# Performance work log

Measured on AMD Instinct MI355X. Metric: run time of the kernel, lower is better.

Reference implementation:

```python
import jax, jax.numpy as jnp
import numpy as np

H_DIM = 64
GRID = 8
NBR = 2.0
BN_EPS = 1e-5
N_SEQ = 64
N_PED = 64
BOTTLENECK = 1024


def setup_inputs() -> dict:
    key = jax.random.key(0)
    k0, k1, k2, k3 = jax.random.split(key, 4)
    batch = N_SEQ * N_PED
    h_states = jax.random.normal(k0, (1, batch, H_DIM), jnp.float32)
    # positions spread over a 4x4 area so some neighbors fall inside the 2.0 neighborhood
    end_pos = jax.random.uniform(k1, (batch, 2), jnp.float32) * 4.0
    rel_pos = jax.random.normal(k2, (batch, 2), jnp.float32)
    starts = jnp.arange(N_SEQ, dtype=jnp.int32) * N_PED
    seq_start_end = jnp.stack([starts, starts + N_PED], axis=1)
    in_dim = GRID * GRID * H_DIM  # 4096
    W = jax.random.normal(k3, (in_dim, BOTTLENECK), jnp.float32) / np.sqrt(in_dim)
    b = jnp.zeros((BOTTLENECK,), jnp.float32)
    gamma = jnp.ones((BOTTLENECK,), jnp.float32)
    beta = jnp.zeros((BOTTLENECK,), jnp.float32)
    return {"h_states": h_states, "seq_start_end": seq_start_end, "end_pos": end_pos,
            "rel_pos": rel_pos, "W": W, "b": b, "gamma": gamma, "beta": beta}


def _pool_scene(hidden, pos):
    # hidden: (n, h), pos: (n, 2). Pair (i, j): ped j binned into ped i's grid.
    n, h = hidden.shape
    g2 = GRID * GRID
    half = NBR / 2.0
    tl_x = pos[:, 0] - half
    tl_y = pos[:, 1] + half
    br_x = pos[:, 0] + half
    br_y = pos[:, 1] - half
    px = pos[None, :, 0]  # (1, n) -> broadcast over i
    py = pos[None, :, 1]
    cell_x = jnp.floor((px - tl_x[:, None]) / NBR * GRID)
    cell_y = jnp.floor((tl_y[:, None] - py) / NBR * GRID)
    grid = (cell_x + cell_y * GRID).astype(jnp.int32) + 1  # slot 0 = trash bin
    oob = ((px >= br_x[:, None]) | (px <= tl_x[:, None]) |
           (py >= tl_y[:, None]) | (py <= br_y[:, None]) |
           jnp.eye(n, dtype=bool))  # self-interaction excluded
    grid = grid + (jnp.arange(n, dtype=jnp.int32) * g2)[:, None]
    grid = jnp.where(oob, 0, grid)  # (n, n)
    src = jnp.broadcast_to(hidden[None], (n, n, h)).reshape(-1, h)
    buf = jnp.zeros((n * g2 + 1, h), hidden.dtype).at[grid.reshape(-1)].add(src)
    return buf[1:].reshape(n, g2 * h)


def reference(h_states, seq_start_end, end_pos, rel_pos, W, b, gamma, beta):
    batch = end_pos.shape[0]
    n_seq = seq_start_end.shape[0]
    n_ped = batch // n_seq  # equal-length scenes by construction
    hid = h_states.reshape(-1, H_DIM).reshape(n_seq, n_ped, H_DIM)
    pos = end_pos.reshape(n_seq, n_ped, 2)
    pool_h = jax.vmap(_pool_scene)(hid, pos).reshape(batch, -1)  # (batch, 4096)
    x = pool_h @ W + b
    # BatchNorm1d in training mode (batch statistics, biased variance)
    mean = jnp.mean(x, axis=0)
    var = jnp.var(x, axis=0)
    x = (x - mean) * jax.lax.rsqrt(var + BN_EPS) * gamma + beta
    return jax.nn.relu(x)
```

## Files before the change

### kernel.cpp

```cpp
#include <hip/hip_runtime.h>
#include <hip/hip_bf16.h>


#define NPED  64
#define BATCH 4096
#define HDIM  64
#define G2    64
#define KDIM  4096
#define NOUT  1024

typedef __attribute__((ext_vector_type(8))) short short8;
typedef __attribute__((ext_vector_type(4))) float f32x4;

__device__ __forceinline__ unsigned short f2bf(float f) {
    __hip_bfloat16 h = __float2bfloat16(f);
    return *reinterpret_cast<unsigned short*>(&h);
}

__device__ __forceinline__ void lds_load16(const void* g, void* l) {
    __builtin_amdgcn_global_load_lds(
        (const __attribute__((address_space(1))) void*)g,
        (__attribute__((address_space(3))) void*)l, 16, 0, 0);
}

__global__ __launch_bounds__(512) void pool_kernel(const float* __restrict__ h,
                                                   const float* __restrict__ pos,
                                                   unsigned short* __restrict__ A2) {
    __shared__ float hs[NPED * HDIM];
    __shared__ float pl[NPED * 2];
    int t = threadIdx.x;
    int w = t >> 6, lane = t & 63;
    int p0 = blockIdx.x * 8;
    int sbase = p0 & ~(NPED - 1);
    if (t < 128) pl[t] = pos[sbase * 2 + t];
    {
        const float4* src = (const float4*)(h + (size_t)sbase * HDIM);
        float4* dst = (float4*)hs;
        dst[t] = src[t];
        dst[t + 512] = src[t + 512];
    }
    __syncthreads();

    int i = p0 + w;
    int il = i & (NPED - 1);
    float cx0 = pl[2 * il], cy0 = pl[2 * il + 1];
    float tlx = cx0 - 1.f, tly = cy0 + 1.f, brx = cx0 + 1.f, bry = cy0 - 1.f;
    float px = pl[2 * lane], py = pl[2 * lane + 1];
    bool inb = (lane != il) && !(px >= brx || px <= tlx || py >= tly || py <= bry);
    int cellx = (int)floorf((px - tlx) * 4.f);
    int celly = (int)floorf((tly - py) * 4.f);
    int cell = cellx + celly * 8;
    inb = inb && ((unsigned)cell < 64u);

    int mtile = i >> 4, r = i & 15;
    unsigned short* outb = A2 + (size_t)mtile * 65536 + r * 8
                              + (lane >> 5) * 512 + ((lane >> 3) & 3) * 128 + (lane & 7);
    const float* hrow = hs + lane;
    #pragma unroll
    for (int c = 0; c < 64; ++c) {
        unsigned long long m = __ballot(inb && (cell == c));
        float a = 0.f;
        while (m) {
            int j = __builtin_ctzll(m);
            m &= m - 1;
            a += hrow[j * HDIM];
        }
        outb[c * 1024] = f2bf(a);
    }
}

__global__ __launch_bounds__(256) void wt_kernel(const float* __restrict__ W,
                                                 unsigned short* __restrict__ Wt,
                                                 float* __restrict__ stats) {
    __shared__ unsigned short tile[64][66];
    int k0 = blockIdx.x * 64;
    int n0 = blockIdx.y * 64;
    int t = threadIdx.x;
    if (blockIdx.x == 0 && blockIdx.y < 8) stats[blockIdx.y * 256 + t] = 0.f;
    #pragma unroll
    for (int p = 0; p < 4; ++p) {
        int lin = p * 256 + t;
        int c4 = lin & 15, kl = lin >> 4;
        float4 v = ((const float4*)(W + (size_t)(k0 + kl) * NOUT + n0))[c4];
        tile[c4 * 4 + 0][kl] = f2bf(v.x);
        tile[c4 * 4 + 1][kl] = f2bf(v.y);
        tile[c4 * 4 + 2][kl] = f2bf(v.z);
        tile[c4 * 4 + 3][kl] = f2bf(v.w);
    }
    __syncthreads();
    unsigned int* out = (unsigned int*)Wt;
    #pragma unroll
    for (int p = 0; p < 8; ++p) {
        int lin = p * 256 + t;
        int ku = lin & 31, nl = lin >> 5;
        unsigned int v = (unsigned int)tile[nl][2 * ku] |
                         ((unsigned int)tile[nl][2 * ku + 1] << 16);
        out[(size_t)(n0 + nl) * (KDIM / 2) + (k0 >> 1) + ku] = v;
    }
}

__global__ __launch_bounds__(256, 2) void gemm_kernel(const unsigned short* __restrict__ A2,
                                                      const unsigned short* __restrict__ Bt,
                                                      float* __restrict__ C,
                                                      float* __restrict__ P1,
                                                      float* __restrict__ P2,
                                                      float* __restrict__ P3) {
    __shared__ __align__(16) unsigned short Bs[128 * 64];
    int t = threadIdx.x;
    int w = t >> 6, lane = t & 63;
    int m0 = blockIdx.x * 256, n0 = blockIdx.y * 128;
    int kbase = blockIdx.z * 1024;
    int wm = w * 64;

    f32x4 acc[4][8];
    #pragma unroll
    for (int i = 0; i < 4; ++i)
        #pragma unroll
        for (int j = 0; j < 8; ++j)
            acc[i][j] = (f32x4){0.f, 0.f, 0.f, 0.f};

    int rbase = w * 32 + (lane >> 3);
    int koff = ((lane & 7) ^ (lane >> 3)) * 8;
    const unsigned short* Bg = Bt + (size_t)(n0 + rbase) * KDIM + kbase + koff;
    unsigned short* BsW = Bs + w * 2048 + lane * 8;

    const unsigned short* Abase = A2 + (size_t)((m0 + wm) >> 4) * 65536 + lane * 8;
    int ktile0 = kbase >> 5;

    for (int kt = 0; kt < 1024; kt += 64) {
        #pragma unroll
        for (int q = 0; q < 4; ++q)
            lds_load16(Bg + (size_t)q * 8 * KDIM + kt, BsW + q * 512);
        short8 af[2][4];
        int ktile = ktile0 + (kt >> 5);
        #pragma unroll
        for (int kk = 0; kk < 2; ++kk)
            #pragma unroll
            for (int i = 0; i < 4; ++i)
                af[kk][i] = *(const short8*)(Abase + ((size_t)i * 128 + ktile + kk) * 512);
        __syncthreads();
        #pragma unroll
        for (int kk = 0; kk < 2; ++kk) {
            int chunk = ((kk * 4 + (lane >> 4)) ^ (lane & 7)) * 8;
            #pragma unroll
            for (int j = 0; j < 8; ++j) {
                short8 b = *(const short8*)&Bs[(j * 16 + (lane & 15)) * 64 + chunk];
                #pragma unroll
                for (int i = 0; i < 4; ++i)
                    acc[i][j] = __builtin_amdgcn_mfma_f32_16x16x32_bf16(af[kk][i], b, acc[i][j], 0, 0, 0);
            }
        }
        __syncthreads();
    }

    float* dst = blockIdx.z == 0 ? C : blockIdx.z == 1 ? P1 : blockIdx.z == 2 ? P2 : P3;
    int col0 = n0 + (lane & 15);
    int row0 = m0 + wm + ((lane >> 4) << 2);
    #pragma unroll
    for (int i = 0; i < 4; ++i)
        #pragma unroll
        for (int j = 0; j < 8; ++j)
            #pragma unroll
            for (int r = 0; r < 4; ++r)
                dst[(size_t)(row0 + i * 16 + r) * NOUT + col0 + j * 16] = acc[i][j][r];
}

__global__ __launch_bounds__(256) void combine_stats(float* __restrict__ C,
                                                     const float* __restrict__ P1,
                                                     const float* __restrict__ P2,
                                                     const float* __restrict__ P3,
                                                     float* __restrict__ stats) {
    int t = threadIdx.x;
    int colchunk = blockIdx.x & 3;
    int rowchunk = blockIdx.x >> 2;
    int col = colchunk * 256 + t;
    size_t base = (size_t)rowchunk * 32 * NOUT + col;
    float s = 0.f, s2 = 0.f;
    #pragma unroll 4
    for (int r = 0; r < 32; ++r) {
        size_t ix = base + (size_t)r * NOUT;
        float v = (C[ix] + P1[ix]) + (P2[ix] + P3[ix]);
        C[ix] = v;
        s += v; s2 += v * v;
    }
    atomicAdd(&stats[col], s);
    atomicAdd(&stats[NOUT + col], s2);
}

__global__ __launch_bounds__(256) void norm_kernel(float* __restrict__ C,
                                                   const float* __restrict__ stats,
                                                   const float* __restrict__ gamma,
                                                   const float* __restrict__ beta) {
    int idx = blockIdx.x * 256 + threadIdx.x;
    int col4 = idx & 255;
    float4 x = ((const float4*)C)[idx];
    float4 s = ((const float4*)stats)[col4];
    float4 q = ((const float4*)(stats + NOUT))[col4];
    float4 g = ((const float4*)gamma)[col4];
    float4 b = ((const float4*)beta)[col4];
    const float inv_n = 1.f / 4096.f;
    float m, inv;
    m = s.x * inv_n; inv = rsqrtf(q.x * inv_n - m * m + 1e-5f); x.x = fmaxf((x.x - m) * inv * g.x + b.x, 0.f);
    m = s.y * inv_n; inv = rsqrtf(q.y * inv_n - m * m + 1e-5f); x.y = fmaxf((x.y - m) * inv * g.y + b.y, 0.f);
    m = s.z * inv_n; inv = rsqrtf(q.z * inv_n - m * m + 1e-5f); x.z = fmaxf((x.z - m) * inv * g.z + b.z, 0.f);
    m = s.w * inv_n; inv = rsqrtf(q.w * inv_n - m * m + 1e-5f); x.w = fmaxf((x.w - m) * inv * g.w + b.w, 0.f);
    ((float4*)C)[idx] = x;
}

extern "C" void kernel_launch(void* const* d_in, const int* in_sizes, int n_in,
                              void* d_out, int out_size, void* d_ws, size_t ws_size,
                              hipStream_t stream) {
    const float* h      = (const float*)d_in[0];
    const float* endpos = (const float*)d_in[2];
    const float* W      = (const float*)d_in[4];
    const float* gamma  = (const float*)d_in[6];
    const float* beta   = (const float*)d_in[7];
    float* C = (float*)d_out;

    char* ws = (char*)d_ws;
    size_t off = 0;
    unsigned short* A2 = (unsigned short*)(ws + off); off += (size_t)BATCH * KDIM * 2;
    unsigned short* Wt = (unsigned short*)(ws + off); off += (size_t)NOUT * KDIM * 2;
    float* P1 = (float*)(ws + off); off += (size_t)BATCH * NOUT * 4;
    float* P2 = (float*)(ws + off); off += (size_t)BATCH * NOUT * 4;
    float* P3 = (float*)(ws + off); off += (size_t)BATCH * NOUT * 4;
    float* stats = (float*)(ws + off);

    pool_kernel<<<BATCH / 8, 512, 0, stream>>>(h, endpos, A2);
    wt_kernel<<<dim3(KDIM / 64, NOUT / 64), 256, 0, stream>>>(W, Wt, stats);
    gemm_kernel<<<dim3(BATCH / 256, NOUT / 128, 4), 256, 0, stream>>>(A2, Wt, C, P1, P2, P3);
    combine_stats<<<512, 256, 0, stream>>>(C, P1, P2, P3, stats);
    norm_kernel<<<(BATCH * NOUT / 4) / 256, 256, 0, stream>>>(C, stats, gamma, beta);
}
```

Before: 149.9 us.

## Rewrite GEMM as double-buffered 256x256 tile pipeline with XCD-aware block mapping

The split-K GEMM moves from 256x128 tiles with 4 waves to 256x256 tiles with 8 waves. Both A and B are now staged into LDS with double buffering, and the next K-tile's global-to-LDS loads are interleaved with the MFMA quadrants under explicit barriers, waitcnts and setprio. A 1D grid with XCD-aware remapping is meant to keep blocks that share operand panels on the same L2. The goal is to hide memory latency and raise operand reuse, at the cost of 128KB of LDS per block and a heavily hand-scheduled, fragile synchronisation sequence.

```diff
diff --git a/kernel.cpp b/kernel.cpp
--- a/kernel.cpp
+++ b/kernel.cpp
@@ -22,6 +22,14 @@
         (const __attribute__((address_space(1))) void*)g,
         (__attribute__((address_space(3))) void*)l, 16, 0, 0);
 }
+
+#define BAR() do { __builtin_amdgcn_sched_barrier(0); \
+                   __builtin_amdgcn_s_barrier(); \
+                   __builtin_amdgcn_sched_barrier(0); } while (0)
+#define LGKM0() do { asm volatile("s_waitcnt lgkmcnt(0)" ::: "memory"); \
+                     __builtin_amdgcn_sched_barrier(0); } while (0)
+#define VMCNT4() asm volatile("s_waitcnt vmcnt(4)" ::: "memory")
+#define VMCNT0() asm volatile("s_waitcnt vmcnt(0)" ::: "memory")
 
 __global__ __launch_bounds__(512) void pool_kernel(const float* __restrict__ h,
                                                    const float* __restrict__ pos,
@@ -99,67 +107,186 @@
     }
 }
 
-__global__ __launch_bounds__(256, 2) void gemm_kernel(const unsigned short* __restrict__ A2,
+
+__device__ __forceinline__ void stage_A_half(const unsigned short* __restrict__ A2blk,
+                                             unsigned short* AsBuf, int T, int h, int t) {
+    #pragma unroll
+    for (int q = 0; q < 2; ++q) {
+        int s = q * 512 + t;
+        int ml = h * 8 + (s >> 7);
+        int inner = s & 127;
+        lds_load16(A2blk + (size_t)ml * 65536 + T * 1024 + inner * 8,
+                   AsBuf + h * 8192 + s * 8);
+    }
+}
+
+__device__ __forceinline__ void stage_B_half(const unsigned short* __restrict__ Wtblk,
+                                             unsigned short* BsBuf, int T, int h, int t) {
+    #pragma unroll
+    for (int q = 0; q < 2; ++q) {
+        int s = q * 512 + t;
+        int row = h * 128 + (s >> 3);
+        int swz = (s & 7) ^ ((s >> 3) & 7);
+        lds_load16(Wtblk + (size_t)row * KDIM + T * 64 + swz * 8,
+                   BsBuf + h * 8192 + s * 8);
+    }
+}
+
+__device__ __forceinline__ void read_A(short8 (&a)[2][4], const unsigned short* AsBuf,
+                                       int mtbase, int lane) {
+    #pragma unroll
+    for (int i = 0; i < 4; ++i)
+        #pragma unroll
+        for (int kk = 0; kk < 2; ++kk)
+            a[kk][i] = *(const short8*)(AsBuf + (mtbase + i) * 1024 + kk * 512 + lane * 8);
+}
+
+__device__ __forceinline__ void read_B(short8 (&b)[2][2], const unsigned short* BsBuf,
+                                       int rowbase, int lane) {
+    #pragma unroll
+    for (int j = 0; j < 2; ++j) {
+        int row = rowbase + j * 16 + (lane & 15);
+        #pragma unroll
+        for (int kk = 0; kk < 2; ++kk)
+            b[kk][j] = *(const short8*)(BsBuf + row * 64 +
+                                        (((kk * 4) + (lane >> 4)) ^ (row & 7)) * 8);
+    }
+}
+
+__device__ __forceinline__ void quad_mfma(f32x4 (&acc)[8][4], const short8 (&a)[2][4],
+                                          const short8 (&b)[2][2], int mh, int nh) {
+    __builtin_amdgcn_s_setprio(1);
+    #pragma unroll
+    for (int kk = 0; kk < 2; ++kk)
+        #pragma unroll
+        for (int i = 0; i < 4; ++i)
+            #pragma unroll
+            for (int j = 0; j < 2; ++j)
+                acc[mh * 4 + i][nh * 2 + j] = __builtin_amdgcn_mfma_f32_16x16x32_bf16(
+                    a[kk][i], b[kk][j], acc[mh * 4 + i][nh * 2 + j], 0, 0, 0);
+    __builtin_amdgcn_s_setprio(0);
+}
+
+__global__ __launch_bounds__(512, 2) void gemm_kernel(const unsigned short* __restrict__ A2,
                                                       const unsigned short* __restrict__ Bt,
                                                       float* __restrict__ C,
                                                       float* __restrict__ P1,
                                                       float* __restrict__ P2,
                                                       float* __restrict__ P3) {
-    __shared__ __align__(16) unsigned short Bs[128 * 64];
+    __shared__ __align__(16) unsigned short sh[65536];
+    unsigned short* As0 = sh;
+    unsigned short* As1 = sh + 16384;
+    unsigned short* Bs0 = sh + 32768;
+    unsigned short* Bs1 = sh + 49152;
+
     int t = threadIdx.x;
     int w = t >> 6, lane = t & 63;
-    int m0 = blockIdx.x * 256, n0 = blockIdx.y * 128;
-    int kbase = blockIdx.z * 1024;
-    int wm = w * 64;
-
-    f32x4 acc[4][8];
-    #pragma unroll
-    for (int i = 0; i < 4; ++i)
-        #pragma unroll
-        for (int j = 0; j < 8; ++j)
+
+    int bid = blockIdx.x;
+    int xcd = bid & 7, slot = bid >> 3;
+    int combo = xcd * 2 + (slot >> 4);
+    int xb = slot & 15, yb = combo & 3, zb = combo >> 2;
+
+    int m0 = xb * 256, n0 = yb * 256;
+    int wm8 = (w >> 2) * 8;
+    int wn64 = (w & 3) * 64;
+
+    const unsigned short* A2blk = A2 + (size_t)(m0 >> 4) * 65536 + (size_t)zb * 16384;
+    const unsigned short* Wtblk = Bt + (size_t)n0 * KDIM + (size_t)zb * 1024;
+
+    f32x4 acc[8][4];
+    #pragma unroll
+    for (int i = 0; i < 8; ++i)
+        #pragma unroll
+        for (int j = 0; j < 4; ++j)
             acc[i][j] = (f32x4){0.f, 0.f, 0.f, 0.f};
 
-    int rbase = w * 32 + (lane >> 3);
-    int koff = ((lane & 7) ^ (lane >> 3)) * 8;
-    const unsigned short* Bg = Bt + (size_t)(n0 + rbase) * KDIM + kbase + koff;
-    unsigned short* BsW = Bs + w * 2048 + lane * 8;
-
-    const unsigned short* Abase = A2 + (size_t)((m0 + wm) >> 4) * 65536 + lane * 8;
-    int ktile0 = kbase >> 5;
-
-    for (int kt = 0; kt < 1024; kt += 64) {
-        #pragma unroll
-        for (int q = 0; q < 4; ++q)
-            lds_load16(Bg + (size_t)q * 8 * KDIM + kt, BsW + q * 512);
-        short8 af[2][4];
-        int ktile = ktile0 + (kt >> 5);
-        #pragma unroll
-        for (int kk = 0; kk < 2; ++kk)
-            #pragma unroll
-            for (int i = 0; i < 4; ++i)
-                af[kk][i] = *(const short8*)(Abase + ((size_t)i * 128 + ktile + kk) * 512);
-        __syncthreads();
-        #pragma unroll
-        for (int kk = 0; kk < 2; ++kk) {
-            int chunk = ((kk * 4 + (lane >> 4)) ^ (lane & 7)) * 8;
-            #pragma unroll
-            for (int j = 0; j < 8; ++j) {
-                short8 b = *(const short8*)&Bs[(j * 16 + (lane & 15)) * 64 + chunk];
-                #pragma unroll
-                for (int i = 0; i < 4; ++i)
-                    acc[i][j] = __builtin_amdgcn_mfma_f32_16x16x32_bf16(af[kk][i], b, acc[i][j], 0, 0, 0);
-            }
-        }
-        __syncthreads();
-    }
-
-    float* dst = blockIdx.z == 0 ? C : blockIdx.z == 1 ? P1 : blockIdx.z == 2 ? P2 : P3;
-    int col0 = n0 + (lane & 15);
-    int row0 = m0 + wm + ((lane >> 4) << 2);
-    #pragma unroll
-    for (int i = 0; i < 4; ++i)
-        #pragma unroll
-        for (int j = 0; j < 8; ++j)
+    short8 aLo[2][4], aHi[2][4], bf[2][2];
+
+    stage_A_half(A2blk, As0, 0, 0, t);
+    stage_A_half(A2blk, As0, 0, 1, t);
+    stage_B_half(Wtblk, Bs0, 0, 0, t);
+    stage_B_half(Wtblk, Bs0, 0, 1, t);
+    stage_A_half(A2blk, As1, 1, 0, t);
+    stage_A_half(A2blk, As1, 1, 1, t);
+    VMCNT4();
+    BAR();
+
+    for (int T = 0; T < 14; T += 2) {
+        read_A(aLo, As0, wm8, lane);
+        read_B(bf, Bs0, wn64, lane);
+        stage_B_half(Wtblk, Bs1, T + 1, 0, t);
+        BAR(); LGKM0(); quad_mfma(acc, aLo, bf, 0, 0); BAR();
+        read_A(aHi, As0, wm8 + 4, lane);
+        read_B(bf, Bs0, wn64 + 32, lane);
+        stage_B_half(Wtblk, Bs1, T + 1, 1, t);
+        BAR(); LGKM0(); quad_mfma(acc, aLo, bf, 0, 1); BAR();
+        read_B(bf, Bs0, wn64, lane);
+        stage_A_half(A2blk, As0, T + 2, 0, t);
+        BAR(); LGKM0(); quad_mfma(acc, aHi, bf, 1, 0); BAR();
+        read_B(bf, Bs0, wn64 + 32, lane);
+        stage_A_half(A2blk, As0, T + 2, 1, t);
+        BAR(); LGKM0(); quad_mfma(acc, aHi, bf, 1, 1);
+        VMCNT4(); BAR();
+
+        read_A(aLo, As1, wm8, lane);
+        read_B(bf, Bs1, wn64, lane);
+        stage_B_half(Wtblk, Bs0, T + 2, 0, t);
+        BAR(); LGKM0(); quad_mfma(acc, aLo, bf, 0, 0); BAR();
+        read_A(aHi, As1, wm8 + 4, lane);
+        read_B(bf, Bs1, wn64 + 32, lane);
+        stage_B_half(Wtblk, Bs0, T + 2, 1, t);
+        BAR(); LGKM0(); quad_mfma(acc, aLo, bf, 0, 1); BAR();
+        read_B(bf, Bs1, wn64, lane);
+        stage_A_half(A2blk, As1, T + 3, 0, t);
+        BAR(); LGKM0(); quad_mfma(acc, aHi, bf, 1, 0); BAR();
+        read_B(bf, Bs1, wn64 + 32, lane);
+        stage_A_half(A2blk, As1, T + 3, 1, t);
+        BAR(); LGKM0(); quad_mfma(acc, aHi, bf, 1, 1);
+        VMCNT4(); BAR();
+    }
+
+    {
+        const int T = 14;
+        read_A(aLo, As0, wm8, lane);
+        read_B(bf, Bs0, wn64, lane);
+        stage_B_half(Wtblk, Bs1, T + 1, 0, t);
+        BAR(); LGKM0(); quad_mfma(acc, aLo, bf, 0, 0); BAR();
+
+        read_A(aHi, As0, wm8 + 4, lane);
+        read_B(bf, Bs0, wn64 + 32, lane);
+        stage_B_half(Wtblk, Bs1, T + 1, 1, t);
+        BAR(); LGKM0(); quad_mfma(acc, aLo, bf, 0, 1); BAR();
+
+        read_B(bf, Bs0, wn64, lane);
+        BAR(); LGKM0(); quad_mfma(acc, aHi, bf, 1, 0); BAR();
+
+        read_B(bf, Bs0, wn64 + 32, lane);
+        BAR(); LGKM0(); quad_mfma(acc, aHi, bf, 1, 1);
+        VMCNT0(); BAR();
+
+        read_A(aLo, As1, wm8, lane);
+        read_B(bf, Bs1, wn64, lane);
+        BAR(); LGKM0(); quad_mfma(acc, aLo, bf, 0, 0); BAR();
+
+        read_A(aHi, As1, wm8 + 4, lane);
+        read_B(bf, Bs1, wn64 + 32, lane);
+        BAR(); LGKM0(); quad_mfma(acc, aLo, bf, 0, 1); BAR();
+
+        read_B(bf, Bs1, wn64, lane);
+        BAR(); LGKM0(); quad_mfma(acc, aHi, bf, 1, 0); BAR();
+
+        read_B(bf, Bs1, wn64 + 32, lane);
+        BAR(); LGKM0(); quad_mfma(acc, aHi, bf, 1, 1);
+    }
+
+    float* dst = zb == 0 ? C : zb == 1 ? P1 : zb == 2 ? P2 : P3;
+    int col0 = n0 + wn64 + (lane & 15);
+    int row0 = m0 + (w >> 2) * 128 + ((lane >> 4) << 2);
+    #pragma unroll
+    for (int i = 0; i < 8; ++i)
+        #pragma unroll
+        for (int j = 0; j < 4; ++j)
             #pragma unroll
             for (int r = 0; r < 4; ++r)
                 dst[(size_t)(row0 + i * 16 + r) * NOUT + col0 + j * 16] = acc[i][j][r];
@@ -228,7 +355,7 @@
 
     pool_kernel<<<BATCH / 8, 512, 0, stream>>>(h, endpos, A2);
     wt_kernel<<<dim3(KDIM / 64, NOUT / 64), 256, 0, stream>>>(W, Wt, stats);
-    gemm_kernel<<<dim3(BATCH / 256, NOUT / 128, 4), 256, 0, stream>>>(A2, Wt, C, P1, P2, P3);
+    gemm_kernel<<<dim3(256), 512, 0, stream>>>(A2, Wt, C, P1, P2, P3);
     combine_stats<<<512, 256, 0, stream>>>(C, P1, P2, P3, stats);
     norm_kernel<<<(BATCH * NOUT / 4) / 256, 256, 0, stream>>>(C, stats, gamma, beta);
 }
```

Measured after the change: 158.4 us. +5.6%, slower.

## Double-buffer GEMM B tiles in LDS with split A prefetch and XCD-aware block mapping

Applied to the files above, without the earlier changes.

Restructures the split-K bf16 GEMM so B tiles are double-buffered in LDS, with the next tile staged through global_load_lds while the current one is consumed. A fragments are split into low and high halves that are prefetched in a ping-pong pattern using explicit vmcnt waits, sched barriers and s_setprio around the MFMA blocks. The wave layout changes from 4x1 to 2x2 (each wave covers 128 rows by 64 columns), which cuts LDS B reads per wave. The 3D grid becomes a 1D grid remapped so each XCD handles nearby tiles for L2 reuse. This aims to hide global and LDS latency behind MFMA work, at the cost of double the LDS use and hand-tuned wait counts that must match the issue order exactly.

```diff
diff --git a/kernel.cpp b/kernel.cpp
--- a/kernel.cpp
+++ b/kernel.cpp
@@ -22,6 +22,12 @@
         (const __attribute__((address_space(1))) void*)g,
         (__attribute__((address_space(3))) void*)l, 16, 0, 0);
 }
+
+#define BAR() do { __builtin_amdgcn_sched_barrier(0); \
+                   __builtin_amdgcn_s_barrier(); \
+                   __builtin_amdgcn_sched_barrier(0); } while (0)
+#define VMCNT(n) do { asm volatile("s_waitcnt vmcnt(" #n ")" ::: "memory"); \
+                      __builtin_amdgcn_sched_barrier(0); } while (0)
 
 __global__ __launch_bounds__(512) void pool_kernel(const float* __restrict__ h,
                                                    const float* __restrict__ pos,
@@ -99,67 +105,155 @@
     }
 }
 
+
+__device__ __forceinline__ void stage_B(const unsigned short* __restrict__ Wtblk,
+                                        unsigned short* BsBuf, int T, int t) {
+    #pragma unroll
+    for (int q = 0; q < 4; ++q) {
+        int s = q * 256 + t;
+        int row = s >> 3;
+        int swz = (s & 7) ^ (row & 7);
+        lds_load16(Wtblk + (size_t)row * KDIM + T * 64 + swz * 8,
+                   BsBuf + s * 8);
+    }
+}
+
 __global__ __launch_bounds__(256, 2) void gemm_kernel(const unsigned short* __restrict__ A2,
                                                       const unsigned short* __restrict__ Bt,
                                                       float* __restrict__ C,
                                                       float* __restrict__ P1,
                                                       float* __restrict__ P2,
                                                       float* __restrict__ P3) {
-    __shared__ __align__(16) unsigned short Bs[128 * 64];
+    __shared__ __align__(16) unsigned short Bs[16384];
+
     int t = threadIdx.x;
     int w = t >> 6, lane = t & 63;
-    int m0 = blockIdx.x * 256, n0 = blockIdx.y * 128;
-    int kbase = blockIdx.z * 1024;
-    int wm = w * 64;
-
-    f32x4 acc[4][8];
+
+    int bid = blockIdx.x;
+    int xcd = bid & 7, slot = bid >> 3;
+    int combo = xcd * 4 + (slot >> 4);
+    int xb = slot & 15, yb = combo & 7, zb = combo >> 3;
+
+    int m0 = xb * 256, n0 = yb * 128;
+    int wn = (w & 1) * 64;
+    int mtbase = (m0 >> 4) + (w >> 1) * 8;
+
+    const unsigned short* Ab = A2 + (size_t)mtbase * 65536
+                                  + (size_t)(zb * 32) * 512 + lane * 8;
+    const unsigned short* Wtblk = Bt + (size_t)n0 * KDIM + (size_t)zb * 1024;
+
+    f32x4 acc[8][4];
+    #pragma unroll
+    for (int i = 0; i < 8; ++i)
+        #pragma unroll
+        for (int j = 0; j < 4; ++j)
+            acc[i][j] = (f32x4){0.f, 0.f, 0.f, 0.f};
+
+    short8 aLo[2][4], aHi[2][4], b[2][4];
+
+    stage_B(Wtblk, Bs, 0, t);
+    __builtin_amdgcn_sched_barrier(0);
     #pragma unroll
     for (int i = 0; i < 4; ++i)
         #pragma unroll
-        for (int j = 0; j < 8; ++j)
-            acc[i][j] = (f32x4){0.f, 0.f, 0.f, 0.f};
-
-    int rbase = w * 32 + (lane >> 3);
-    int koff = ((lane & 7) ^ (lane >> 3)) * 8;
-    const unsigned short* Bg = Bt + (size_t)(n0 + rbase) * KDIM + kbase + koff;
-    unsigned short* BsW = Bs + w * 2048 + lane * 8;
-
-    const unsigned short* Abase = A2 + (size_t)((m0 + wm) >> 4) * 65536 + lane * 8;
-    int ktile0 = kbase >> 5;
-
-    for (int kt = 0; kt < 1024; kt += 64) {
-        #pragma unroll
-        for (int q = 0; q < 4; ++q)
-            lds_load16(Bg + (size_t)q * 8 * KDIM + kt, BsW + q * 512);
-        short8 af[2][4];
-        int ktile = ktile0 + (kt >> 5);
+        for (int kk = 0; kk < 2; ++kk)
+            aLo[kk][i] = *(const short8*)(Ab + (size_t)i * 65536 + (size_t)kk * 512);
+    VMCNT(8);
+    BAR();
+
+    for (int T = 0; T < 15; ++T) {
+        const unsigned short* Bsr = Bs + (T & 1) * 8192;
+        unsigned short* Bsw = Bs + ((T & 1) ^ 1) * 8192;
+        #pragma unroll
+        for (int j = 0; j < 4; ++j) {
+            int rB = wn + j * 16 + (lane & 15);
+            #pragma unroll
+            for (int kk = 0; kk < 2; ++kk)
+                b[kk][j] = *(const short8*)(Bsr + rB * 64 +
+                                            (((kk * 4 + (lane >> 4)) ^ (rB & 7)) * 8));
+        }
+        #pragma unroll
+        for (int i = 0; i < 4; ++i)
+            #pragma unroll
+            for (int kk = 0; kk < 2; ++kk)
+                aHi[kk][i] = *(const short8*)(Ab + (size_t)(i + 4) * 65536 +
+                                              (size_t)(T * 2 + kk) * 512);
+        stage_B(Wtblk, Bsw, T + 1, t);
+        VMCNT(12);
+        __builtin_amdgcn_s_setprio(1);
         #pragma unroll
         for (int kk = 0; kk < 2; ++kk)
             #pragma unroll
             for (int i = 0; i < 4; ++i)
-                af[kk][i] = *(const short8*)(Abase + ((size_t)i * 128 + ktile + kk) * 512);
-        __syncthreads();
-        #pragma unroll
-        for (int kk = 0; kk < 2; ++kk) {
-            int chunk = ((kk * 4 + (lane >> 4)) ^ (lane & 7)) * 8;
-            #pragma unroll
-            for (int j = 0; j < 8; ++j) {
-                short8 b = *(const short8*)&Bs[(j * 16 + (lane & 15)) * 64 + chunk];
                 #pragma unroll
-                for (int i = 0; i < 4; ++i)
-                    acc[i][j] = __builtin_amdgcn_mfma_f32_16x16x32_bf16(af[kk][i], b, acc[i][j], 0, 0, 0);
-            }
+                for (int j = 0; j < 4; ++j)
+                    acc[i][j] = __builtin_amdgcn_mfma_f32_16x16x32_bf16(
+                        aLo[kk][i], b[kk][j], acc[i][j], 0, 0, 0);
+        __builtin_amdgcn_s_setprio(0);
+        BAR();
+        #pragma unroll
+        for (int i = 0; i < 4; ++i)
+            #pragma unroll
+            for (int kk = 0; kk < 2; ++kk)
+                aLo[kk][i] = *(const short8*)(Ab + (size_t)i * 65536 +
+                                              (size_t)((T + 1) * 2 + kk) * 512);
+        VMCNT(8);
+        __builtin_amdgcn_s_setprio(1);
+        #pragma unroll
+        for (int kk = 0; kk < 2; ++kk)
+            #pragma unroll
+            for (int i = 0; i < 4; ++i)
+                #pragma unroll
+                for (int j = 0; j < 4; ++j)
+                    acc[i + 4][j] = __builtin_amdgcn_mfma_f32_16x16x32_bf16(
+                        aHi[kk][i], b[kk][j], acc[i + 4][j], 0, 0, 0);
+        __builtin_amdgcn_s_setprio(0);
+        BAR();
+    }
+
+    {
+        const unsigned short* Bsr = Bs + 8192;
+        #pragma unroll
+        for (int j = 0; j < 4; ++j) {
+            int rB = wn + j * 16 + (lane & 15);
+            #pragma unroll
+            for (int kk = 0; kk < 2; ++kk)
+                b[kk][j] = *(const short8*)(Bsr + rB * 64 +
+                                            (((kk * 4 + (lane >> 4)) ^ (rB & 7)) * 8));
         }
-        __syncthreads();
-    }
-
-    float* dst = blockIdx.z == 0 ? C : blockIdx.z == 1 ? P1 : blockIdx.z == 2 ? P2 : P3;
-    int col0 = n0 + (lane & 15);
-    int row0 = m0 + wm + ((lane >> 4) << 2);
-    #pragma unroll
-    for (int i = 0; i < 4; ++i)
-        #pragma unroll
-        for (int j = 0; j < 8; ++j)
+        #pragma unroll
+        for (int i = 0; i < 4; ++i)
+            #pragma unroll
+            for (int kk = 0; kk < 2; ++kk)
+                aHi[kk][i] = *(const short8*)(Ab + (size_t)(i + 4) * 65536 +
+                                              (size_t)(15 * 2 + kk) * 512);
+        VMCNT(8);
+        #pragma unroll
+        for (int kk = 0; kk < 2; ++kk)
+            #pragma unroll
+            for (int i = 0; i < 4; ++i)
+                #pragma unroll
+                for (int j = 0; j < 4; ++j)
+                    acc[i][j] = __builtin_amdgcn_mfma_f32_16x16x32_bf16(
+                        aLo[kk][i], b[kk][j], acc[i][j], 0, 0, 0);
+        VMCNT(0);
+        #pragma unroll
+        for (int kk = 0; kk < 2; ++kk)
+            #pragma unroll
+            for (int i = 0; i < 4; ++i)
+                #pragma unroll
+                for (int j = 0; j < 4; ++j)
+                    acc[i + 4][j] = __builtin_amdgcn_mfma_f32_16x16x32_bf16(
+                        aHi[kk][i], b[kk][j], acc[i + 4][j], 0, 0, 0);
+    }
+
+    float* dst = zb == 0 ? C : zb == 1 ? P1 : zb == 2 ? P2 : P3;
+    int col0 = n0 + wn + (lane & 15);
+    int row0 = m0 + (w >> 1) * 128 + ((lane >> 4) << 2);
+    #pragma unroll
+    for (int i = 0; i < 8; ++i)
+        #pragma unroll
+        for (int j = 0; j < 4; ++j)
             #pragma unroll
             for (int r = 0; r < 4; ++r)
                 dst[(size_t)(row0 + i * 16 + r) * NOUT + col0 + j * 16] = acc[i][j][r];
@@ -228,7 +322,7 @@
 
     pool_kernel<<<BATCH / 8, 512, 0, stream>>>(h, endpos, A2);
     wt_kernel<<<dim3(KDIM / 64, NOUT / 64), 256, 0, stream>>>(W, Wt, stats);
-    gemm_kernel<<<dim3(BATCH / 256, NOUT / 128, 4), 256, 0, stream>>>(A2, Wt, C, P1, P2, P3);
+    gemm_kernel<<<dim3(512), 256, 0, stream>>>(A2, Wt, C, P1, P2, P3);
     combine_stats<<<512, 256, 0, stream>>>(C, P1, P2, P3, stats);
     norm_kernel<<<(BATCH * NOUT / 4) / 256, 256, 0, stream>>>(C, stats, gamma, beta);
 }
```

New measurement: 157.4 us. 1.05x slower.

## Replace global split-K partials with in-block split-K reduction and fused BN stats

Applied to the files above, without the earlier changes.

The GEMM no longer splits K across four grid slices that write full fp32 partial outputs to global memory for a separate combine kernel. Each 512-thread block now computes a 128x128 tile and splits K between two 256-thread halves, reducing the halves through LDS. Per-column sum and sum-of-squares are computed in the epilogue and pushed out with atomics. This removes three 16 MB partial buffers and the combine_stats launch. The cost is fewer blocks (256), 64 KB of LDS per block, and a smaller per-wave tile.

```diff
diff --git a/kernel.cpp b/kernel.cpp
--- a/kernel.cpp
+++ b/kernel.cpp
@@ -99,92 +99,106 @@
     }
 }
 
-__global__ __launch_bounds__(256, 2) void gemm_kernel(const unsigned short* __restrict__ A2,
+
+__global__ __launch_bounds__(512, 2) void gemm_kernel(const unsigned short* __restrict__ A2,
                                                       const unsigned short* __restrict__ Bt,
                                                       float* __restrict__ C,
-                                                      float* __restrict__ P1,
-                                                      float* __restrict__ P2,
-                                                      float* __restrict__ P3) {
-    __shared__ __align__(16) unsigned short Bs[128 * 64];
+                                                      float* __restrict__ stats) {
+    __shared__ __align__(16) char shmem[65536];
+    unsigned short* Bs = (unsigned short*)shmem;
+
     int t = threadIdx.x;
     int w = t >> 6, lane = t & 63;
-    int m0 = blockIdx.x * 256, n0 = blockIdx.y * 128;
-    int kbase = blockIdx.z * 1024;
-    int wm = w * 64;
-
-    f32x4 acc[4][8];
+    int kh = w >> 2, wsub = w & 3;
+
+    int bid = blockIdx.x;
+    int yb = bid & 7, xb = bid >> 3;
+    int m0 = xb * 128, n0 = yb * 128;
+    int wm = (wsub >> 1) * 64, wn = (wsub & 1) * 64;
+
+    const unsigned short* Ab = A2 + (size_t)((m0 >> 4) + (wm >> 4)) * 65536 + lane * 8;
+    const unsigned short* Wtb = Bt + (size_t)n0 * KDIM;
+
+    int kh_t = t >> 8, tt = t & 255;
+
+    f32x4 acc[4][4];
     #pragma unroll
     for (int i = 0; i < 4; ++i)
         #pragma unroll
-        for (int j = 0; j < 8; ++j)
+        for (int j = 0; j < 4; ++j)
             acc[i][j] = (f32x4){0.f, 0.f, 0.f, 0.f};
 
-    int rbase = w * 32 + (lane >> 3);
-    int koff = ((lane & 7) ^ (lane >> 3)) * 8;
-    const unsigned short* Bg = Bt + (size_t)(n0 + rbase) * KDIM + kbase + koff;
-    unsigned short* BsW = Bs + w * 2048 + lane * 8;
-
-    const unsigned short* Abase = A2 + (size_t)((m0 + wm) >> 4) * 65536 + lane * 8;
-    int ktile0 = kbase >> 5;
-
-    for (int kt = 0; kt < 1024; kt += 64) {
-        #pragma unroll
-        for (int q = 0; q < 4; ++q)
-            lds_load16(Bg + (size_t)q * 8 * KDIM + kt, BsW + q * 512);
+    for (int sk = 0; sk < 32; ++sk) {
+        #pragma unroll
+        for (int q = 0; q < 4; ++q) {
+            int s = q * 256 + tt;
+            int row = s >> 3;
+            int swz = (s & 7) ^ (row & 7);
+            lds_load16(Wtb + (size_t)row * KDIM + kh_t * 2048 + sk * 64 + swz * 8,
+                       Bs + kh_t * 8192 + s * 8);
+        }
         short8 af[2][4];
-        int ktile = ktile0 + (kt >> 5);
         #pragma unroll
         for (int kk = 0; kk < 2; ++kk)
             #pragma unroll
             for (int i = 0; i < 4; ++i)
-                af[kk][i] = *(const short8*)(Abase + ((size_t)i * 128 + ktile + kk) * 512);
+                af[kk][i] = *(const short8*)(Ab + (size_t)i * 65536 +
+                                             (size_t)(kh * 64 + sk * 2 + kk) * 512);
         __syncthreads();
+        const unsigned short* Bsr = Bs + kh * 8192;
         #pragma unroll
         for (int kk = 0; kk < 2; ++kk) {
-            int chunk = ((kk * 4 + (lane >> 4)) ^ (lane & 7)) * 8;
-            #pragma unroll
-            for (int j = 0; j < 8; ++j) {
-                short8 b = *(const short8*)&Bs[(j * 16 + (lane & 15)) * 64 + chunk];
+            #pragma unroll
+            for (int j = 0; j < 4; ++j) {
+                int rB = wn + j * 16 + (lane & 15);
+                short8 b = *(const short8*)(Bsr + rB * 64 +
+                               (((kk * 4 + (lane >> 4)) ^ (rB & 7)) * 8));
                 #pragma unroll
                 for (int i = 0; i < 4; ++i)
-                    acc[i][j] = __builtin_amdgcn_mfma_f32_16x16x32_bf16(af[kk][i], b, acc[i][j], 0, 0, 0);
+                    acc[i][j] = __builtin_amdgcn_mfma_f32_16x16x32_bf16(
+                        af[kk][i], b, acc[i][j], 0, 0, 0);
             }
         }
         __syncthreads();
     }
 
-    float* dst = blockIdx.z == 0 ? C : blockIdx.z == 1 ? P1 : blockIdx.z == 2 ? P2 : P3;
-    int col0 = n0 + (lane & 15);
-    int row0 = m0 + wm + ((lane >> 4) << 2);
-    #pragma unroll
-    for (int i = 0; i < 4; ++i)
-        #pragma unroll
-        for (int j = 0; j < 8; ++j)
-            #pragma unroll
-            for (int r = 0; r < 4; ++r)
-                dst[(size_t)(row0 + i * 16 + r) * NOUT + col0 + j * 16] = acc[i][j][r];
-}
-
-__global__ __launch_bounds__(256) void combine_stats(float* __restrict__ C,
-                                                     const float* __restrict__ P1,
-                                                     const float* __restrict__ P2,
-                                                     const float* __restrict__ P3,
-                                                     float* __restrict__ stats) {
-    int t = threadIdx.x;
-    int colchunk = blockIdx.x & 3;
-    int rowchunk = blockIdx.x >> 2;
-    int col = colchunk * 256 + t;
-    size_t base = (size_t)rowchunk * 32 * NOUT + col;
-    float s = 0.f, s2 = 0.f;
-    #pragma unroll 4
-    for (int r = 0; r < 32; ++r) {
-        size_t ix = base + (size_t)r * NOUT;
-        float v = (C[ix] + P1[ix]) + (P2[ix] + P3[ix]);
-        C[ix] = v;
-        s += v; s2 += v * v;
-    }
-    atomicAdd(&stats[col], s);
-    atomicAdd(&stats[NOUT + col], s2);
+    f32x4* red = (f32x4*)shmem;
+    if (kh == 1) {
+        #pragma unroll
+        for (int i = 0; i < 4; ++i)
+            #pragma unroll
+            for (int j = 0; j < 4; ++j)
+                red[(i * 4 + j) * 256 + tt] = acc[i][j];
+    }
+    __syncthreads();
+    if (kh == 0) {
+        #pragma unroll
+        for (int i = 0; i < 4; ++i)
+            #pragma unroll
+            for (int j = 0; j < 4; ++j)
+                acc[i][j] += red[(i * 4 + j) * 256 + t];
+
+        int col0 = n0 + wn + (lane & 15);
+        int row0 = m0 + wm + ((lane >> 4) << 2);
+        #pragma unroll
+        for (int j = 0; j < 4; ++j) {
+            float s = 0.f, s2 = 0.f;
+            #pragma unroll
+            for (int i = 0; i < 4; ++i)
+                #pragma unroll
+                for (int r = 0; r < 4; ++r) {
+                    float v = acc[i][j][r];
+                    C[(size_t)(row0 + i * 16 + r) * NOUT + col0 + j * 16] = v;
+                    s += v; s2 += v * v;
+                }
+            s  += __shfl_xor(s, 16);  s  += __shfl_xor(s, 32);
+            s2 += __shfl_xor(s2, 16); s2 += __shfl_xor(s2, 32);
+            if (lane < 16) {
+                atomicAdd(&stats[col0 + j * 16], s);
+                atomicAdd(&stats[NOUT + col0 + j * 16], s2);
+            }
+        }
+    }
 }
 
 __global__ __launch_bounds__(256) void norm_kernel(float* __restrict__ C,
@@ -221,14 +235,10 @@
     size_t off = 0;
     unsigned short* A2 = (unsigned short*)(ws + off); off += (size_t)BATCH * KDIM * 2;
     unsigned short* Wt = (unsigned short*)(ws + off); off += (size_t)NOUT * KDIM * 2;
-    float* P1 = (float*)(ws + off); off += (size_t)BATCH * NOUT * 4;
-    float* P2 = (float*)(ws + off); off += (size_t)BATCH * NOUT * 4;
-    float* P3 = (float*)(ws + off); off += (size_t)BATCH * NOUT * 4;
     float* stats = (float*)(ws + off);
 
     pool_kernel<<<BATCH / 8, 512, 0, stream>>>(h, endpos, A2);
     wt_kernel<<<dim3(KDIM / 64, NOUT / 64), 256, 0, stream>>>(W, Wt, stats);
-    gemm_kernel<<<dim3(BATCH / 256, NOUT / 128, 4), 256, 0, stream>>>(A2, Wt, C, P1, P2, P3);
-    combine_stats<<<512, 256, 0, stream>>>(C, P1, P2, P3, stats);
+    gemm_kernel<<<dim3(256), 512, 0, stream>>>(A2, Wt, C, stats);
     norm_kernel<<<(BATCH * NOUT / 4) / 256, 256, 0, stream>>>(C, stats, gamma, beta);
 }
```

New measurement: 164.1 us. +9.4%, slower.
